# Optimization experiments

Hardware: AMD Instinct MI355X
Metric: run time of the kernel (lower is better)

Reference implementation:

```python
import jax, jax.numpy as jnp
import numpy as np

D_MODEL = 512
N_HEADS = 8
D_HEAD = D_MODEL // N_HEADS
SCALE = D_HEAD ** -0.5


def _rel_shift(x):
    # x: (b, h, qlen, klen) -> Transformer-XL relative shift
    b, h, qlen, klen = x.shape
    x = jnp.pad(x, ((0, 0), (0, 0), (0, 0), (1, 0)))        # (b,h,q,k+1)
    x = x.reshape(b, h, klen + 1, qlen)
    x = x[:, :, 1:, :].reshape(b, h, qlen, klen)
    return x


def setup_inputs() -> dict:
    key = jax.random.key(0)
    ks = jax.random.split(key, 12)
    B, S = 2, 2048
    P = 2 * S - 1
    w = lambda k, shape: (jax.random.normal(k, shape, jnp.float32) * 0.02)
    return {
        "x": jax.random.normal(ks[0], (B, S, D_MODEL), jnp.float32),
        "pos_emb": jax.random.normal(ks[1], (P, D_MODEL), jnp.float32),
        "Wq": w(ks[2], (D_MODEL, D_MODEL)), "bq": jnp.zeros((D_MODEL,), jnp.float32),
        "Wk": w(ks[3], (D_MODEL, D_MODEL)), "bk": jnp.zeros((D_MODEL,), jnp.float32),
        "Wv": w(ks[4], (D_MODEL, D_MODEL)), "bv": jnp.zeros((D_MODEL,), jnp.float32),
        "Wp": w(ks[5], (D_MODEL, D_MODEL)),
        "Wo": w(ks[6], (D_MODEL, D_MODEL)), "bo": jnp.zeros((D_MODEL,), jnp.float32),
        "pos_bias_u": w(ks[7], (N_HEADS, D_HEAD)),
        "pos_bias_v": w(ks[8], (N_HEADS, D_HEAD)),
    }


def reference(x, pos_emb, Wq, bq, Wk, bk, Wv, bv, Wp, Wo, bo, pos_bias_u, pos_bias_v):
    B, S, _ = x.shape
    # projections (torch Linear: y = x @ W^T + b; here W stored as (in, out))
    q = (x @ Wq + bq).reshape(B, S, N_HEADS, D_HEAD)
    k = (x @ Wk + bk).reshape(B, S, N_HEADS, D_HEAD)
    v = (x @ Wv + bv).reshape(B, S, N_HEADS, D_HEAD)
    p = (pos_emb @ Wp).reshape(-1, N_HEADS, D_HEAD)  # (2S-1, H, D)

    # content score: (q + u) @ k^T  -> (B,H,S,S)
    content = jnp.einsum("bshd,bthd->bhst", q + pos_bias_u, k)
    # position score: (q + v_bias) @ p^T -> (B,H,S,2S-1), then rel_shift
    pos = jnp.einsum("bshd,phd->bhsp", q + pos_bias_v, p)
    pos = _rel_shift(pos)[..., :S]  # trim to kv_len

    attn = jax.nn.softmax((content + pos) * SCALE, axis=-1)
    out = jnp.einsum("bhst,bthd->bshd", attn, v).reshape(B, S, D_MODEL)
    out = out @ Wo + bo
    return out
```

## Files before the change

kernel.cpp:

```cpp
#include <hip/hip_runtime.h>

#define DM    512
#define NH    8
#define DH    64
#define SEQ   2048
#define PLEN  4095
#define NB    2
#define ATT_SCALE 0.125f

typedef __attribute__((ext_vector_type(8))) _Float16 half8;
typedef __attribute__((ext_vector_type(4))) float   floatx4;

__global__ __launch_bounds__(256)
void cast16(const float* __restrict__ s0, _Float16* __restrict__ d0, long n0,
            const float* __restrict__ s1, _Float16* __restrict__ d1, long n1)
{
    const float* src = blockIdx.y ? s1 : s0;
    _Float16* dst = blockIdx.y ? d1 : d0;
    const long n = blockIdx.y ? n1 : n0;
    const long i = ((long)blockIdx.x * 256 + threadIdx.x) * 8;
    if (i >= n) return;
    float4 f0 = *(const float4*)(src + i);
    float4 f1 = *(const float4*)(src + i + 4);
    half8 o;
    o[0] = (_Float16)f0.x; o[1] = (_Float16)f0.y;
    o[2] = (_Float16)f0.z; o[3] = (_Float16)f0.w;
    o[4] = (_Float16)f1.x; o[5] = (_Float16)f1.y;
    o[6] = (_Float16)f1.z; o[7] = (_Float16)f1.w;
    *(half8*)(dst + i) = o;
}

__global__ __launch_bounds__(256)
void pack_w(const float* __restrict__ W0, const float* __restrict__ W1,
            const float* __restrict__ W2, const float* __restrict__ W3,
            const float* __restrict__ W4, _Float16* __restrict__ Wt)
{
    __shared__ _Float16 tile[64 * 72];
    const int z = blockIdx.z;
    const float* W = (z == 0) ? W0 : (z == 1) ? W1 : (z == 2) ? W2
                   : (z == 3) ? W3 : W4;
    _Float16* dst_base = Wt + (size_t)z * DM * DM;

    const int n0 = blockIdx.x * 64, k0 = blockIdx.y * 64;
    const int t = threadIdx.x;
    {
        const int kr = t >> 2, nch = (t & 3) * 16;
        const float* src = W + (size_t)(k0 + kr) * DM + n0 + nch;
        float4 f0 = *(const float4*)(src + 0);
        float4 f1 = *(const float4*)(src + 4);
        float4 f2 = *(const float4*)(src + 8);
        float4 f3 = *(const float4*)(src + 12);
        _Float16* trow = &tile[kr * 72 + nch];
        trow[0]  = (_Float16)f0.x; trow[1]  = (_Float16)f0.y;
        trow[2]  = (_Float16)f0.z; trow[3]  = (_Float16)f0.w;
        trow[4]  = (_Float16)f1.x; trow[5]  = (_Float16)f1.y;
        trow[6]  = (_Float16)f1.z; trow[7]  = (_Float16)f1.w;
        trow[8]  = (_Float16)f2.x; trow[9]  = (_Float16)f2.y;
        trow[10] = (_Float16)f2.z; trow[11] = (_Float16)f2.w;
        trow[12] = (_Float16)f3.x; trow[13] = (_Float16)f3.y;
        trow[14] = (_Float16)f3.z; trow[15] = (_Float16)f3.w;
    }
    __syncthreads();
    {
        const int nr = t >> 2, kch = (t & 3) * 16;
        half8 o0, o1;
#pragma unroll
        for (int i = 0; i < 8; ++i) o0[i] = tile[(kch + i) * 72 + nr];
#pragma unroll
        for (int i = 0; i < 8; ++i) o1[i] = tile[(kch + 8 + i) * 72 + nr];
        _Float16* dst = dst_base + (size_t)(n0 + nr) * DM + k0 + kch;
        *(half8*)dst = o0;
        *(half8*)(dst + 8) = o1;
    }
}

__global__ __launch_bounds__(256)
void gemm_qkv(const _Float16* __restrict__ A, const _Float16* __restrict__ Wt,
              const float* __restrict__ bq, const float* __restrict__ bk,
              const float* __restrict__ bv, const float* __restrict__ bu,
              const float* __restrict__ bvb,
              _Float16* __restrict__ qu16, _Float16* __restrict__ qv16,
              _Float16* __restrict__ k16, _Float16* __restrict__ vt16)
{
    __shared__ _Float16 aS[64 * 72];
    __shared__ _Float16 wS[64 * 72];

    const int t = threadIdx.x;
    const int w = t >> 6, lane = t & 63, quad = lane >> 4, l16 = lane & 15;
    const int z = blockIdx.z;
    const int n0 = blockIdx.x * 64;
    const int m0 = blockIdx.y * 64;
    const int srow = t >> 2, sch = (t & 3) * 16;
    const _Float16* Wz = Wt + (size_t)z * DM * DM;

    floatx4 acc[4];
#pragma unroll
    for (int ct = 0; ct < 4; ++ct) acc[ct] = (floatx4){0.f, 0.f, 0.f, 0.f};

    for (int k0 = 0; k0 < DM; k0 += 64) {
        __syncthreads();
        {
            const _Float16* asrc = A + (size_t)(m0 + srow) * DM + k0 + sch;
            *(half8*)&aS[srow * 72 + sch]     = *(const half8*)asrc;
            *(half8*)&aS[srow * 72 + sch + 8] = *(const half8*)(asrc + 8);
            const _Float16* wsrc = Wz + (size_t)(n0 + srow) * DM + k0 + sch;
            *(half8*)&wS[srow * 72 + sch]     = *(const half8*)wsrc;
            *(half8*)&wS[srow * 72 + sch + 8] = *(const half8*)(wsrc + 8);
        }
        __syncthreads();
#pragma unroll
        for (int kb = 0; kb < 2; ++kb) {
            half8 af = *(const half8*)&aS[(16 * w + l16) * 72 + kb * 32 + quad * 8];
#pragma unroll
            for (int ct = 0; ct < 4; ++ct) {
                half8 bf = *(const half8*)&wS[(16 * ct + l16) * 72 + kb * 32 + quad * 8];
                acc[ct] = __builtin_amdgcn_mfma_f32_16x16x32_f16(af, bf, acc[ct], 0, 0, 0);
            }
        }
    }

    const int h = n0 >> 6;
    if (z == 0) {
#pragma unroll
        for (int ct = 0; ct < 4; ++ct) {
            const int n = n0 + 16 * ct + l16;
            const float bval = bq[n], uval = bu[n], vval = bvb[n];
#pragma unroll
            for (int r = 0; r < 4; ++r) {
                const int m = m0 + 16 * w + 4 * quad + r;
                const int b = m >> 11, s = m & 2047;
                const size_t dst = ((size_t)((h * NB + b) * SEQ) + s) * DH + (n & 63);
                const float q = acc[ct][r] + bval;
                qu16[dst] = (_Float16)((q + uval) * ATT_SCALE);
                qv16[dst] = (_Float16)((q + vval) * ATT_SCALE);
            }
        }
    } else if (z == 1) {
#pragma unroll
        for (int ct = 0; ct < 4; ++ct) {
            const int n = n0 + 16 * ct + l16;
            const float bval = bk[n];
#pragma unroll
            for (int r = 0; r < 4; ++r) {
                const int m = m0 + 16 * w + 4 * quad + r;
                const int b = m >> 11, s = m & 2047;
                k16[((size_t)((h * NB + b) * SEQ) + s) * DH + (n & 63)] =
                    (_Float16)(acc[ct][r] + bval);
            }
        }
    } else {
        __syncthreads();
#pragma unroll
        for (int ct = 0; ct < 4; ++ct) {
            const float bval = bv[n0 + 16 * ct + l16];
#pragma unroll
            for (int r = 0; r < 4; ++r)
                aS[(16 * w + 4 * quad + r) * 72 + 16 * ct + l16] =
                    (_Float16)(acc[ct][r] + bval);
        }
        __syncthreads();
        const int b = m0 >> 11, s0 = m0 & 2047;
        const int drow = t >> 2;
        half8 o0, o1;
#pragma unroll
        for (int i = 0; i < 8; ++i) o0[i] = aS[(sch + i) * 72 + drow];
#pragma unroll
        for (int i = 0; i < 8; ++i) o1[i] = aS[(sch + 8 + i) * 72 + drow];
        _Float16* dst = vt16 + ((size_t)((h * NB + b) * DH) + drow) * SEQ + s0 + sch;
        *(half8*)dst = o0;
        *(half8*)(dst + 8) = o1;
    }
}

template<int MODE>
__global__ __launch_bounds__(256)
void gemm_mfma(const _Float16* __restrict__ A, const _Float16* __restrict__ Wt,
               const float* __restrict__ bias, void* __restrict__ out0, int M)
{
    __shared__ _Float16 aS[64 * 72];
    __shared__ _Float16 wS[64 * 72];

    const int t = threadIdx.x;
    const int w = t >> 6, lane = t & 63, quad = lane >> 4, l16 = lane & 15;
    const int n0 = blockIdx.x * 64;
    const int m0 = blockIdx.y * 64;
    const int srow = t >> 2, sch = (t & 3) * 16;

    floatx4 acc[4];
#pragma unroll
    for (int ct = 0; ct < 4; ++ct) acc[ct] = (floatx4){0.f, 0.f, 0.f, 0.f};

    for (int k0 = 0; k0 < DM; k0 += 64) {
        __syncthreads();
        if (MODE != 4 || m0 + srow < M) {
            const _Float16* asrc = A + (size_t)(m0 + srow) * DM + k0 + sch;
            *(half8*)&aS[srow * 72 + sch]     = *(const half8*)asrc;
            *(half8*)&aS[srow * 72 + sch + 8] = *(const half8*)(asrc + 8);
        } else {
            half8 z = {};
            *(half8*)&aS[srow * 72 + sch]     = z;
            *(half8*)&aS[srow * 72 + sch + 8] = z;
        }
        {
            const _Float16* wsrc = Wt + (size_t)(n0 + srow) * DM + k0 + sch;
            *(half8*)&wS[srow * 72 + sch]     = *(const half8*)wsrc;
            *(half8*)&wS[srow * 72 + sch + 8] = *(const half8*)(wsrc + 8);
        }
        __syncthreads();
#pragma unroll
        for (int kb = 0; kb < 2; ++kb) {
            half8 af = *(const half8*)&aS[(16 * w + l16) * 72 + kb * 32 + quad * 8];
#pragma unroll
            for (int ct = 0; ct < 4; ++ct) {
                half8 bf = *(const half8*)&wS[(16 * ct + l16) * 72 + kb * 32 + quad * 8];
                acc[ct] = __builtin_amdgcn_mfma_f32_16x16x32_f16(af, bf, acc[ct], 0, 0, 0);
            }
        }
    }

    if (MODE == 0) {
        float* O = (float*)out0;
#pragma unroll
        for (int ct = 0; ct < 4; ++ct) {
            const int n = n0 + 16 * ct + l16;
            const float bval = bias[n];
#pragma unroll
            for (int r = 0; r < 4; ++r) {
                const int m = m0 + 16 * w + 4 * quad + r;
                O[(size_t)m * DM + n] = acc[ct][r] + bval;
            }
        }
    } else {
        _Float16* po = (_Float16*)out0;
        const int h = n0 >> 6;
#pragma unroll
        for (int ct = 0; ct < 4; ++ct) {
            const int n = n0 + 16 * ct + l16;
#pragma unroll
            for (int r = 0; r < 4; ++r) {
                const int m = m0 + 16 * w + 4 * quad + r;
                if (m < M)
                    po[((size_t)h * PLEN + m) * DH + (n & 63)] = (_Float16)acc[ct][r];
            }
        }
    }
}

__global__ __launch_bounds__(256, 2)
void relattn_mfma(const _Float16* __restrict__ QU,
                  const _Float16* __restrict__ QV,
                  const _Float16* __restrict__ Kp,
                  const _Float16* __restrict__ VT,
                  const _Float16* __restrict__ Pp,
                  _Float16* __restrict__ Out)
{
    __shared__ _Float16 kS[64 * 72];
    __shared__ _Float16 pS[128 * 72];
    __shared__ _Float16 vS[64 * 72];
    __shared__ _Float16 tS[64 * 88];

    const int t = threadIdx.x;
    const int w = t >> 6, lane = t & 63, quad = lane >> 4, l16 = lane & 15;
    const int i0 = blockIdx.x * 64;
    const int h = blockIdx.y, b = blockIdx.z;
    const size_t hb = (size_t)(h * NB + b);
    const int cbase = 48 - 16 * w;

    half8 qa[2], va[2];
    {
        const _Float16* qrow = QU + (hb * SEQ + i0 + 16 * w + l16) * DH + quad * 8;
        const _Float16* vrow = QV + (hb * SEQ + i0 + 16 * w + l16) * DH + quad * 8;
        qa[0] = *(const half8*)qrow;       qa[1] = *(const half8*)(qrow + 32);
        va[0] = *(const half8*)vrow;       va[1] = *(const half8*)(vrow + 32);
    }

    floatx4 O[4];
    float lsum[4] = {0.f, 0.f, 0.f, 0.f};
#pragma unroll
    for (int ct = 0; ct < 4; ++ct) O[ct] = (floatx4){0.f, 0.f, 0.f, 0.f};

    const int srow = t >> 2, schunk = (t & 3) * 16;
    const int prow = t >> 1, pch = (t & 1) * 32;

    const _Float16* Kbase = Kp + hb * SEQ * DH;
    const _Float16* Vbase = VT + hb * DH * SEQ;
    const _Float16* Pbase = Pp + (size_t)h * PLEN * DH;

    for (int j0 = 0; j0 < SEQ; j0 += 64) {
        __syncthreads();

        {
            const _Float16* src = Kbase + (size_t)(j0 + srow) * DH + schunk;
            half8 a0 = *(const half8*)src;
            half8 a1 = *(const half8*)(src + 8);
            *(half8*)&kS[srow * 72 + schunk] = a0;
            *(half8*)&kS[srow * 72 + schunk + 8] = a1;
            const _Float16* vsrc = Vbase + (size_t)srow * SEQ + j0 + schunk;
            half8 b0 = *(const half8*)vsrc;
            half8 b1 = *(const half8*)(vsrc + 8);
            *(half8*)&vS[srow * 72 + schunk] = b0;
            *(half8*)&vS[srow * 72 + schunk + 8] = b1;
        }
        {
            const int rbase = (SEQ - 1) + j0 - i0 - 63;
            if (prow < 127) {
                const _Float16* psrc = Pbase + (size_t)(rbase + prow) * DH + pch;
                half8 p0 = *(const half8*)(psrc + 0);
                half8 p1 = *(const half8*)(psrc + 8);
                half8 p2 = *(const half8*)(psrc + 16);
                half8 p3 = *(const half8*)(psrc + 24);
                *(half8*)&pS[prow * 72 + pch + 0]  = p0;
                *(half8*)&pS[prow * 72 + pch + 8]  = p1;
                *(half8*)&pS[prow * 72 + pch + 16] = p2;
                *(half8*)&pS[prow * 72 + pch + 24] = p3;
            }
        }
        __syncthreads();

        {
            floatx4 Tacc[5];
#pragma unroll
            for (int c2 = 0; c2 < 5; ++c2) Tacc[c2] = (floatx4){0.f, 0.f, 0.f, 0.f};
#pragma unroll
            for (int kb = 0; kb < 2; ++kb) {
#pragma unroll
                for (int c2 = 0; c2 < 5; ++c2) {
                    half8 bf = *(const half8*)&pS[(cbase + 16 * c2 + l16) * 72 + kb * 32 + quad * 8];
                    Tacc[c2] = __builtin_amdgcn_mfma_f32_16x16x32_f16(va[kb], bf, Tacc[c2], 0, 0, 0);
                }
            }
#pragma unroll
            for (int c2 = 0; c2 < 5; ++c2)
#pragma unroll
                for (int r = 0; r < 4; ++r)
                    tS[(16 * w + 4 * quad + r) * 88 + 16 * c2 + l16] = (_Float16)Tacc[c2][r];
        }
        asm volatile("" ::: "memory");

        floatx4 Sc[4];
#pragma unroll
        for (int ct = 0; ct < 4; ++ct) Sc[ct] = (floatx4){0.f, 0.f, 0.f, 0.f};
#pragma unroll
        for (int kb = 0; kb < 2; ++kb) {
#pragma unroll
            for (int ct = 0; ct < 4; ++ct) {
                half8 bf = *(const half8*)&kS[(16 * ct + l16) * 72 + kb * 32 + quad * 8];
                Sc[ct] = __builtin_amdgcn_mfma_f32_16x16x32_f16(qa[kb], bf, Sc[ct], 0, 0, 0);
            }
        }
#pragma unroll
        for (int ct = 0; ct < 4; ++ct)
#pragma unroll
            for (int r = 0; r < 4; ++r) {
                const int il16 = 4 * quad + r;
                const int c = 16 * ct + l16 - il16 + 15;
                const float e = __expf(Sc[ct][r] +
                                       (float)tS[(16 * w + il16) * 88 + c]);
                Sc[ct][r] = e;
                lsum[r] += e;
            }
        asm volatile("" ::: "memory");

#pragma unroll
        for (int ct = 0; ct < 4; ++ct)
#pragma unroll
            for (int r = 0; r < 4; ++r)
                tS[(16 * w + 4 * quad + r) * 88 + 16 * ct + l16] = (_Float16)Sc[ct][r];
        asm volatile("" ::: "memory");

#pragma unroll
        for (int kb = 0; kb < 2; ++kb) {
            half8 af = *(const half8*)&tS[(16 * w + l16) * 88 + kb * 32 + quad * 8];
#pragma unroll
            for (int ct = 0; ct < 4; ++ct) {
                half8 bf = *(const half8*)&vS[(16 * ct + l16) * 72 + kb * 32 + quad * 8];
                O[ct] = __builtin_amdgcn_mfma_f32_16x16x32_f16(af, bf, O[ct], 0, 0, 0);
            }
        }
        asm volatile("" ::: "memory");
    }

#pragma unroll
    for (int r = 0; r < 4; ++r) {
#pragma unroll
        for (int m = 1; m < 16; m <<= 1) lsum[r] += __shfl_xor(lsum[r], m);
        const float inv = 1.f / lsum[r];
        _Float16* orow = Out + (size_t)(b * SEQ + i0 + 16 * w + 4 * quad + r) * DM + h * DH;
#pragma unroll
        for (int ct = 0; ct < 4; ++ct)
            orow[16 * ct + l16] = (_Float16)(O[ct][r] * inv);
    }
}

extern "C" void kernel_launch(void* const* d_in, const int* in_sizes, int n_in,
                              void* d_out, int out_size, void* d_ws, size_t ws_size,
                              hipStream_t stream)
{
    (void)in_sizes; (void)n_in; (void)out_size; (void)ws_size;
    const float* x   = (const float*)d_in[0];
    const float* pe  = (const float*)d_in[1];
    const float* Wq  = (const float*)d_in[2];
    const float* bq  = (const float*)d_in[3];
    const float* Wk  = (const float*)d_in[4];
    const float* bk  = (const float*)d_in[5];
    const float* Wv  = (const float*)d_in[6];
    const float* bv  = (const float*)d_in[7];
    const float* Wp  = (const float*)d_in[8];
    const float* Wo  = (const float*)d_in[9];
    const float* bo  = (const float*)d_in[10];
    const float* pbu = (const float*)d_in[11];
    const float* pbv = (const float*)d_in[12];
    float* out = (float*)d_out;

    const size_t nX  = (size_t)NB * SEQ * DM;
    const size_t nPe = (size_t)PLEN * DM;
    const size_t nW  = (size_t)DM * DM;
    const size_t nH  = (size_t)NH * NB * SEQ * DH;
    const size_t nPh = (size_t)NH * PLEN * DH;

    _Float16* x16  = (_Float16*)d_ws;
    _Float16* pe16 = x16 + nX;
    _Float16* wt   = pe16 + nPe;
    _Float16* qu16 = wt + 5 * nW;
    _Float16* qv16 = qu16 + nH;
    _Float16* k16  = qv16 + nH;
    _Float16* vt16 = k16 + nH;
    _Float16* p16  = vt16 + nH;
    _Float16* ow16 = p16 + nPh;

    dim3 blk(256);
    cast16<<<dim3(1024, 2), blk, 0, stream>>>(x, x16, (long)nX, pe, pe16, (long)nPe);
    pack_w<<<dim3(8, 8, 5), blk, 0, stream>>>(Wq, Wk, Wv, Wp, Wo, wt);

    gemm_qkv<<<dim3(8, 64, 3), blk, 0, stream>>>(x16, wt, bq, bk, bv, pbu, pbv,
                                                 qu16, qv16, k16, vt16);
    gemm_mfma<4><<<dim3(8, 64), blk, 0, stream>>>(pe16, wt + 3 * nW, nullptr,
                                                  p16, PLEN);

    relattn_mfma<<<dim3(SEQ / 64, NH, NB), blk, 0, stream>>>(
        qu16, qv16, k16, vt16, p16, ow16);

    gemm_mfma<0><<<dim3(8, 64), blk, 0, stream>>>(ow16, wt + 4 * nW, bo,
                                                  out, NB * SEQ);
}
```

Baseline: 203.5 us.

## Split attention over key span, fuse prep/projection kernels, merge partials in output GEMM

Merges the cast and weight-pack kernels into one prep launch, and folds the positional projection into the QKV GEMM launch. The attention kernel now splits the key range into two halves across extra blocks and writes unnormalized fp32 partial outputs and row sums. The final output GEMM combines the two partials, normalizes, casts to fp16 and applies Wo. The attention kernel's occupancy hint is raised and the positional and content MFMAs are interleaved. This trades more grid parallelism and fewer launches for extra fp32 partial traffic. The split has no max-subtraction, matching the earlier softmax path.

```diff
diff --git a/kernel.cpp b/kernel.cpp
--- a/kernel.cpp
+++ b/kernel.cpp
@@ -6,43 +6,47 @@
 #define SEQ   2048
 #define PLEN  4095
 #define NB    2
+#define NSPLIT 2
+#define JSPAN (SEQ / NSPLIT)
 #define ATT_SCALE 0.125f
 
 typedef __attribute__((ext_vector_type(8))) _Float16 half8;
 typedef __attribute__((ext_vector_type(4))) float   floatx4;
 
 __global__ __launch_bounds__(256)
-void cast16(const float* __restrict__ s0, _Float16* __restrict__ d0, long n0,
-            const float* __restrict__ s1, _Float16* __restrict__ d1, long n1)
-{
-    const float* src = blockIdx.y ? s1 : s0;
-    _Float16* dst = blockIdx.y ? d1 : d0;
-    const long n = blockIdx.y ? n1 : n0;
-    const long i = ((long)blockIdx.x * 256 + threadIdx.x) * 8;
-    if (i >= n) return;
-    float4 f0 = *(const float4*)(src + i);
-    float4 f1 = *(const float4*)(src + i + 4);
-    half8 o;
-    o[0] = (_Float16)f0.x; o[1] = (_Float16)f0.y;
-    o[2] = (_Float16)f0.z; o[3] = (_Float16)f0.w;
-    o[4] = (_Float16)f1.x; o[5] = (_Float16)f1.y;
-    o[6] = (_Float16)f1.z; o[7] = (_Float16)f1.w;
-    *(half8*)(dst + i) = o;
-}
-
-__global__ __launch_bounds__(256)
-void pack_w(const float* __restrict__ W0, const float* __restrict__ W1,
-            const float* __restrict__ W2, const float* __restrict__ W3,
-            const float* __restrict__ W4, _Float16* __restrict__ Wt)
+void prep(const float* __restrict__ x, const float* __restrict__ pe,
+          const float* __restrict__ W0, const float* __restrict__ W1,
+          const float* __restrict__ W2, const float* __restrict__ W3,
+          const float* __restrict__ W4,
+          _Float16* __restrict__ x16, _Float16* __restrict__ pe16,
+          _Float16* __restrict__ Wt)
 {
     __shared__ _Float16 tile[64 * 72];
     const int z = blockIdx.z;
-    const float* W = (z == 0) ? W0 : (z == 1) ? W1 : (z == 2) ? W2
-                   : (z == 3) ? W3 : W4;
-    _Float16* dst_base = Wt + (size_t)z * DM * DM;
-
-    const int n0 = blockIdx.x * 64, k0 = blockIdx.y * 64;
     const int t = threadIdx.x;
+
+    if (z < 2) {
+        const float* src = z ? pe : x;
+        _Float16* dst = z ? pe16 : x16;
+        const long n = z ? (long)PLEN * DM : (long)NB * SEQ * DM;
+        const long i = ((long)blockIdx.x * 256 + t) * 8;
+        if (i >= n) return;
+        float4 f0 = *(const float4*)(src + i);
+        float4 f1 = *(const float4*)(src + i + 4);
+        half8 o;
+        o[0] = (_Float16)f0.x; o[1] = (_Float16)f0.y;
+        o[2] = (_Float16)f0.z; o[3] = (_Float16)f0.w;
+        o[4] = (_Float16)f1.x; o[5] = (_Float16)f1.y;
+        o[6] = (_Float16)f1.z; o[7] = (_Float16)f1.w;
+        *(half8*)(dst + i) = o;
+        return;
+    }
+    if (blockIdx.x >= 64) return;
+    const int wz = z - 2;
+    const float* W = (wz == 0) ? W0 : (wz == 1) ? W1 : (wz == 2) ? W2
+                   : (wz == 3) ? W3 : W4;
+    _Float16* dst_base = Wt + (size_t)wz * DM * DM;
+    const int n0 = (blockIdx.x & 7) * 64, k0 = (blockIdx.x >> 3) * 64;
     {
         const int kr = t >> 2, nch = (t & 3) * 16;
         const float* src = W + (size_t)(k0 + kr) * DM + n0 + nch;
@@ -75,12 +79,14 @@
 }
 
 __global__ __launch_bounds__(256)
-void gemm_qkv(const _Float16* __restrict__ A, const _Float16* __restrict__ Wt,
-              const float* __restrict__ bq, const float* __restrict__ bk,
-              const float* __restrict__ bv, const float* __restrict__ bu,
-              const float* __restrict__ bvb,
-              _Float16* __restrict__ qu16, _Float16* __restrict__ qv16,
-              _Float16* __restrict__ k16, _Float16* __restrict__ vt16)
+void gemm_qkvp(const _Float16* __restrict__ X, const _Float16* __restrict__ Pe,
+               const _Float16* __restrict__ Wt,
+               const float* __restrict__ bq, const float* __restrict__ bk,
+               const float* __restrict__ bv, const float* __restrict__ bu,
+               const float* __restrict__ bvb,
+               _Float16* __restrict__ qu16, _Float16* __restrict__ qv16,
+               _Float16* __restrict__ k16, _Float16* __restrict__ vt16,
+               _Float16* __restrict__ p16)
 {
     __shared__ _Float16 aS[64 * 72];
     __shared__ _Float16 wS[64 * 72];
@@ -91,6 +97,7 @@
     const int n0 = blockIdx.x * 64;
     const int m0 = blockIdx.y * 64;
     const int srow = t >> 2, sch = (t & 3) * 16;
+    const _Float16* A = (z == 3) ? Pe : X;
     const _Float16* Wz = Wt + (size_t)z * DM * DM;
 
     floatx4 acc[4];
@@ -99,10 +106,16 @@
 
     for (int k0 = 0; k0 < DM; k0 += 64) {
         __syncthreads();
-        {
+        if (z != 3 || m0 + srow < PLEN) {
             const _Float16* asrc = A + (size_t)(m0 + srow) * DM + k0 + sch;
             *(half8*)&aS[srow * 72 + sch]     = *(const half8*)asrc;
             *(half8*)&aS[srow * 72 + sch + 8] = *(const half8*)(asrc + 8);
+        } else {
+            half8 zz = {};
+            *(half8*)&aS[srow * 72 + sch]     = zz;
+            *(half8*)&aS[srow * 72 + sch + 8] = zz;
+        }
+        {
             const _Float16* wsrc = Wz + (size_t)(n0 + srow) * DM + k0 + sch;
             *(half8*)&wS[srow * 72 + sch]     = *(const half8*)wsrc;
             *(half8*)&wS[srow * 72 + sch + 8] = *(const half8*)(wsrc + 8);
@@ -148,7 +161,7 @@
                     (_Float16)(acc[ct][r] + bval);
             }
         }
-    } else {
+    } else if (z == 2) {
         __syncthreads();
 #pragma unroll
         for (int ct = 0; ct < 4; ++ct) {
@@ -169,90 +182,27 @@
         _Float16* dst = vt16 + ((size_t)((h * NB + b) * DH) + drow) * SEQ + s0 + sch;
         *(half8*)dst = o0;
         *(half8*)(dst + 8) = o1;
-    }
-}
-
-template<int MODE>
-__global__ __launch_bounds__(256)
-void gemm_mfma(const _Float16* __restrict__ A, const _Float16* __restrict__ Wt,
-               const float* __restrict__ bias, void* __restrict__ out0, int M)
-{
-    __shared__ _Float16 aS[64 * 72];
-    __shared__ _Float16 wS[64 * 72];
-
-    const int t = threadIdx.x;
-    const int w = t >> 6, lane = t & 63, quad = lane >> 4, l16 = lane & 15;
-    const int n0 = blockIdx.x * 64;
-    const int m0 = blockIdx.y * 64;
-    const int srow = t >> 2, sch = (t & 3) * 16;
-
-    floatx4 acc[4];
-#pragma unroll
-    for (int ct = 0; ct < 4; ++ct) acc[ct] = (floatx4){0.f, 0.f, 0.f, 0.f};
-
-    for (int k0 = 0; k0 < DM; k0 += 64) {
-        __syncthreads();
-        if (MODE != 4 || m0 + srow < M) {
-            const _Float16* asrc = A + (size_t)(m0 + srow) * DM + k0 + sch;
-            *(half8*)&aS[srow * 72 + sch]     = *(const half8*)asrc;
-            *(half8*)&aS[srow * 72 + sch + 8] = *(const half8*)(asrc + 8);
-        } else {
-            half8 z = {};
-            *(half8*)&aS[srow * 72 + sch]     = z;
-            *(half8*)&aS[srow * 72 + sch + 8] = z;
-        }
-        {
-            const _Float16* wsrc = Wt + (size_t)(n0 + srow) * DM + k0 + sch;
-            *(half8*)&wS[srow * 72 + sch]     = *(const half8*)wsrc;
-            *(half8*)&wS[srow * 72 + sch + 8] = *(const half8*)(wsrc + 8);
-        }
-        __syncthreads();
-#pragma unroll
-        for (int kb = 0; kb < 2; ++kb) {
-            half8 af = *(const half8*)&aS[(16 * w + l16) * 72 + kb * 32 + quad * 8];
-#pragma unroll
-            for (int ct = 0; ct < 4; ++ct) {
-                half8 bf = *(const half8*)&wS[(16 * ct + l16) * 72 + kb * 32 + quad * 8];
-                acc[ct] = __builtin_amdgcn_mfma_f32_16x16x32_f16(af, bf, acc[ct], 0, 0, 0);
-            }
-        }
-    }
-
-    if (MODE == 0) {
-        float* O = (float*)out0;
+    } else {
 #pragma unroll
         for (int ct = 0; ct < 4; ++ct) {
             const int n = n0 + 16 * ct + l16;
-            const float bval = bias[n];
 #pragma unroll
             for (int r = 0; r < 4; ++r) {
                 const int m = m0 + 16 * w + 4 * quad + r;
-                O[(size_t)m * DM + n] = acc[ct][r] + bval;
-            }
-        }
-    } else {
-        _Float16* po = (_Float16*)out0;
-        const int h = n0 >> 6;
-#pragma unroll
-        for (int ct = 0; ct < 4; ++ct) {
-            const int n = n0 + 16 * ct + l16;
-#pragma unroll
-            for (int r = 0; r < 4; ++r) {
-                const int m = m0 + 16 * w + 4 * quad + r;
-                if (m < M)
-                    po[((size_t)h * PLEN + m) * DH + (n & 63)] = (_Float16)acc[ct][r];
+                if (m < PLEN)
+                    p16[((size_t)h * PLEN + m) * DH + (n & 63)] = (_Float16)acc[ct][r];
             }
         }
     }
 }
 
-__global__ __launch_bounds__(256, 2)
+__global__ __launch_bounds__(256, 3)
 void relattn_mfma(const _Float16* __restrict__ QU,
                   const _Float16* __restrict__ QV,
                   const _Float16* __restrict__ Kp,
                   const _Float16* __restrict__ VT,
                   const _Float16* __restrict__ Pp,
-                  _Float16* __restrict__ Out)
+                  float* __restrict__ Opart, float* __restrict__ Lpart)
 {
     __shared__ _Float16 kS[64 * 72];
     __shared__ _Float16 pS[128 * 72];
@@ -262,7 +212,9 @@
     const int t = threadIdx.x;
     const int w = t >> 6, lane = t & 63, quad = lane >> 4, l16 = lane & 15;
     const int i0 = blockIdx.x * 64;
-    const int h = blockIdx.y, b = blockIdx.z;
+    const int h = blockIdx.y;
+    const int b = blockIdx.z & (NB - 1);
+    const int split = blockIdx.z >> 1;
     const size_t hb = (size_t)(h * NB + b);
     const int cbase = 48 - 16 * w;
 
@@ -286,7 +238,8 @@
     const _Float16* Vbase = VT + hb * DH * SEQ;
     const _Float16* Pbase = Pp + (size_t)h * PLEN * DH;
 
-    for (int j0 = 0; j0 < SEQ; j0 += 64) {
+    const int jbeg = split * JSPAN, jend = jbeg + JSPAN;
+    for (int j0 = jbeg; j0 < jend; j0 += 64) {
         __syncthreads();
 
         {
@@ -317,37 +270,31 @@
         }
         __syncthreads();
 
-        {
-            floatx4 Tacc[5];
-#pragma unroll
-            for (int c2 = 0; c2 < 5; ++c2) Tacc[c2] = (floatx4){0.f, 0.f, 0.f, 0.f};
-#pragma unroll
-            for (int kb = 0; kb < 2; ++kb) {
-#pragma unroll
-                for (int c2 = 0; c2 < 5; ++c2) {
-                    half8 bf = *(const half8*)&pS[(cbase + 16 * c2 + l16) * 72 + kb * 32 + quad * 8];
-                    Tacc[c2] = __builtin_amdgcn_mfma_f32_16x16x32_f16(va[kb], bf, Tacc[c2], 0, 0, 0);
-                }
-            }
-#pragma unroll
-            for (int c2 = 0; c2 < 5; ++c2)
-#pragma unroll
-                for (int r = 0; r < 4; ++r)
-                    tS[(16 * w + 4 * quad + r) * 88 + 16 * c2 + l16] = (_Float16)Tacc[c2][r];
-        }
-        asm volatile("" ::: "memory");
-
-        floatx4 Sc[4];
+        floatx4 Tacc[5], Sc[4];
+#pragma unroll
+        for (int c2 = 0; c2 < 5; ++c2) Tacc[c2] = (floatx4){0.f, 0.f, 0.f, 0.f};
 #pragma unroll
         for (int ct = 0; ct < 4; ++ct) Sc[ct] = (floatx4){0.f, 0.f, 0.f, 0.f};
 #pragma unroll
         for (int kb = 0; kb < 2; ++kb) {
+#pragma unroll
+            for (int c2 = 0; c2 < 5; ++c2) {
+                half8 bf = *(const half8*)&pS[(cbase + 16 * c2 + l16) * 72 + kb * 32 + quad * 8];
+                Tacc[c2] = __builtin_amdgcn_mfma_f32_16x16x32_f16(va[kb], bf, Tacc[c2], 0, 0, 0);
+            }
 #pragma unroll
             for (int ct = 0; ct < 4; ++ct) {
                 half8 bf = *(const half8*)&kS[(16 * ct + l16) * 72 + kb * 32 + quad * 8];
                 Sc[ct] = __builtin_amdgcn_mfma_f32_16x16x32_f16(qa[kb], bf, Sc[ct], 0, 0, 0);
             }
         }
+#pragma unroll
+        for (int c2 = 0; c2 < 5; ++c2)
+#pragma unroll
+            for (int r = 0; r < 4; ++r)
+                tS[(16 * w + 4 * quad + r) * 88 + 16 * c2 + l16] = (_Float16)Tacc[c2][r];
+        asm volatile("" ::: "memory");
+
 #pragma unroll
         for (int ct = 0; ct < 4; ++ct)
 #pragma unroll
@@ -384,11 +331,97 @@
     for (int r = 0; r < 4; ++r) {
 #pragma unroll
         for (int m = 1; m < 16; m <<= 1) lsum[r] += __shfl_xor(lsum[r], m);
-        const float inv = 1.f / lsum[r];
-        _Float16* orow = Out + (size_t)(b * SEQ + i0 + 16 * w + 4 * quad + r) * DM + h * DH;
+        const int row = i0 + 16 * w + 4 * quad + r;
+        float* orow = Opart + ((size_t)split * NB * SEQ + b * SEQ + row) * DM + h * DH;
 #pragma unroll
         for (int ct = 0; ct < 4; ++ct)
-            orow[16 * ct + l16] = (_Float16)(O[ct][r] * inv);
+            orow[16 * ct + l16] = O[ct][r];
+        if (l16 == 0)
+            Lpart[((size_t)split * NH * NB + hb) * SEQ + row] = lsum[r];
+    }
+}
+
+__global__ __launch_bounds__(256)
+void gemm_final(const float* __restrict__ Opart, const float* __restrict__ Lpart,
+                const _Float16* __restrict__ Wt, const float* __restrict__ bias,
+                float* __restrict__ Out)
+{
+    __shared__ _Float16 aS[64 * 72];
+    __shared__ _Float16 wS[64 * 72];
+    __shared__ float invS[8][64];
+
+    const int t = threadIdx.x;
+    const int w = t >> 6, lane = t & 63, quad = lane >> 4, l16 = lane & 15;
+    const int n0 = blockIdx.x * 64;
+    const int m0 = blockIdx.y * 64;
+    const int srow = t >> 2, sch = (t & 3) * 16;
+    const int b = m0 >> 11, s0 = m0 & 2047;
+
+#pragma unroll
+    for (int i = t; i < 512; i += 256) {
+        const int hh = i >> 6, rr = i & 63;
+        const size_t base = ((size_t)hh * NB + b) * SEQ + s0 + rr;
+        const float l = Lpart[base] + Lpart[(size_t)NH * NB * SEQ + base];
+        invS[hh][rr] = 1.f / l;
+    }
+
+    floatx4 acc[4];
+#pragma unroll
+    for (int ct = 0; ct < 4; ++ct) acc[ct] = (floatx4){0.f, 0.f, 0.f, 0.f};
+
+    for (int k0 = 0; k0 < DM; k0 += 64) {
+        __syncthreads();
+        {
+            const size_t aoff = ((size_t)b * SEQ + s0 + srow) * DM + k0 + sch;
+            const float* a0 = Opart + aoff;
+            const float* a1 = Opart + (size_t)NB * SEQ * DM + aoff;
+            const float inv = invS[k0 >> 6][srow];
+            half8 o0, o1;
+#pragma unroll
+            for (int c4 = 0; c4 < 2; ++c4) {
+                float4 x0 = *(const float4*)(a0 + c4 * 4);
+                float4 y0 = *(const float4*)(a1 + c4 * 4);
+                o0[c4 * 4 + 0] = (_Float16)((x0.x + y0.x) * inv);
+                o0[c4 * 4 + 1] = (_Float16)((x0.y + y0.y) * inv);
+                o0[c4 * 4 + 2] = (_Float16)((x0.z + y0.z) * inv);
+                o0[c4 * 4 + 3] = (_Float16)((x0.w + y0.w) * inv);
+            }
+#pragma unroll
+            for (int c4 = 0; c4 < 2; ++c4) {
+                float4 x0 = *(const float4*)(a0 + 8 + c4 * 4);
+                float4 y0 = *(const float4*)(a1 + 8 + c4 * 4);
+                o1[c4 * 4 + 0] = (_Float16)((x0.x + y0.x) * inv);
+                o1[c4 * 4 + 1] = (_Float16)((x0.y + y0.y) * inv);
+                o1[c4 * 4 + 2] = (_Float16)((x0.z + y0.z) * inv);
+                o1[c4 * 4 + 3] = (_Float16)((x0.w + y0.w) * inv);
+            }
+            *(half8*)&aS[srow * 72 + sch]     = o0;
+            *(half8*)&aS[srow * 72 + sch + 8] = o1;
+            const _Float16* wsrc = Wt + (size_t)(n0 + srow) * DM + k0 + sch;
+            *(half8*)&wS[srow * 72 + sch]     = *(const half8*)wsrc;
+            *(half8*)&wS[srow * 72 + sch + 8] = *(const half8*)(wsrc + 8);
+        }
+        __syncthreads();
+#pragma unroll
+        for (int kb = 0; kb < 2; ++kb) {
+            half8 af = *(const half8*)&aS[(16 * w + l16) * 72 + kb * 32 + quad * 8];
+#pragma unroll
+            for (int ct = 0; ct < 4; ++ct) {
+                half8 bf = *(const half8*)&wS[(16 * ct + l16) * 72 + kb * 32 + quad * 8];
+                acc[ct] = __builtin_amdgcn_mfma_f32_16x16x32_f16(af, bf, acc[ct], 0, 0, 0);
+            }
+        }
+    }
+
+#pragma unroll
+    for (int ct = 0; ct < 4; ++ct) {
+        const int n = n0 + 16 * ct + l16;
+        const float bval = bias[n];
+#pragma unroll
+        for (int r = 0; r < 4; ++r) {
+            const int m = m0 + 16 * w + 4 * quad + r;
+            Out[(size_t)m * DM + n] = acc[ct][r] + bval;
+        }
     }
 }
 
@@ -426,20 +459,17 @@
     _Float16* k16  = qv16 + nH;
     _Float16* vt16 = k16 + nH;
     _Float16* p16  = vt16 + nH;
-    _Float16* ow16 = p16 + nPh;
+    float* Opart   = (float*)(p16 + nPh);
+    float* Lpart   = Opart + (size_t)NSPLIT * NB * SEQ * DM;
 
     dim3 blk(256);
-    cast16<<<dim3(1024, 2), blk, 0, stream>>>(x, x16, (long)nX, pe, pe16, (long)nPe);
-    pack_w<<<dim3(8, 8, 5), blk, 0, stream>>>(Wq, Wk, Wv, Wp, Wo, wt);
-
-    gemm_qkv<<<dim3(8, 64, 3), blk, 0, stream>>>(x16, wt, bq, bk, bv, pbu, pbv,
-                                                 qu16, qv16, k16, vt16);
-    gemm_mfma<4><<<dim3(8, 64), blk, 0, stream>>>(pe16, wt + 3 * nW, nullptr,
-                                                  p16, PLEN);
-
-    relattn_mfma<<<dim3(SEQ / 64, NH, NB), blk, 0, stream>>>(
-        qu16, qv16, k16, vt16, p16, ow16);
-
-    gemm_mfma<0><<<dim3(8, 64), blk, 0, stream>>>(ow16, wt + 4 * nW, bo,
-                                                  out, NB * SEQ);
+    prep<<<dim3(1024, 1, 7), blk, 0, stream>>>(x, pe, Wq, Wk, Wv, Wp, Wo,
+                                               x16, pe16, wt);
+    gemm_qkvp<<<dim3(8, 64, 4), blk, 0, stream>>>(x16, pe16, wt,
+                                                  bq, bk, bv, pbu, pbv,
+                                                  qu16, qv16, k16, vt16, p16);
+    relattn_mfma<<<dim3(SEQ / 64, NH, NB * NSPLIT), blk, 0, stream>>>(
+        qu16, qv16, k16, vt16, p16, Opart, Lpart);
+    gemm_final<<<dim3(8, 64), blk, 0, stream>>>(Opart, Lpart, wt + 4 * nW, bo,
+                                                out);
 }
```

Measured after the change: 214.9 us. 1.06x slower.
